# Kernel tuning notes

Hardware: AMD Instinct MI355X
Metric: run time of the kernel (lower is better)

The kernel has to match this reference:

```python
import jax, jax.numpy as jnp
import numpy as np

# Action space: 3 discrete action types, 8 options each (MultiDiscrete nvec)
ACTION_NUMS = np.array([8, 8, 8])
A_TOTAL = int(ACTION_NUMS.sum())          # 24
START_IDX = np.cumsum([0, *ACTION_NUMS[:-1]])  # [0, 8, 16]
F, N, D = 4096, 64, 256                   # frames, agents(actions per frame), feat_size
HID = 140                                 # fixed in ForwardNet


def setup_inputs() -> dict:
    key = jax.random.key(0)
    ks = jax.random.split(key, 8)
    s = lambda fan_in: 1.0 / np.sqrt(fan_in)
    return {
        "current_feature": jax.random.normal(ks[0], (F, N, D), jnp.float32),
        "next_feature": jax.random.normal(ks[1], (F, N, D), jnp.float32),
        "actions": jax.random.randint(ks[2], (F, 3, N), 0, 8, dtype=jnp.int32),
        "W1": jax.random.normal(ks[3], (D + A_TOTAL, HID), jnp.float32) * s(D + A_TOTAL),
        "b1": jnp.zeros((HID,), jnp.float32),
        "W2": jax.random.normal(ks[4], (HID, D), jnp.float32) * s(HID),
        "b2": jnp.zeros((D,), jnp.float32),
        "Wi": jax.random.normal(ks[5], (2 * D, A_TOTAL), jnp.float32) * s(2 * D),
        "bi": jnp.zeros((A_TOTAL,), jnp.float32),
    }


def actions2onehot(actions):
    # actions: [F, T, N] int. Vectorized replacement for the triple Python loop:
    # each (frame, agent) row gets a 1 at START_IDX[type] + action, per type.
    start = jnp.asarray(START_IDX, actions.dtype)          # [T]
    idx = actions + start[None, :, None]                    # [F, T, N]
    oh = jax.nn.one_hot(idx, A_TOTAL, dtype=jnp.float32)    # [F, T, N, A]
    return oh.sum(axis=1)                                   # [F, N, A] (column ranges disjoint)


def reference(current_feature, next_feature, actions, W1, b1, W2, b2, Wi, bi):
    action_one_hot = actions2onehot(actions)                       # [F, N, 24]
    # Forward dynamics (attn_target != ICM branch)
    fwd_in = jnp.concatenate([current_feature, action_one_hot], axis=2)  # [F, N, 280]
    h = jax.nn.leaky_relu(fwd_in @ W1 + b1, negative_slope=0.1)
    next_feature_pred = h @ W2 + b2                                # [F, N, 256]
    # Inverse dynamics
    inv_in = jnp.concatenate([current_feature, next_feature], axis=2)   # [F, N, 512]
    action_pred = inv_in @ Wi + bi                                 # [F, N, 24] per-type logits concatenated
    return next_feature_pred, action_pred
```

## Files before the change

kernel.cpp:

```cpp
#include <hip/hip_runtime.h>
#include <hip/hip_bf16.h>
#include <stdint.h>


typedef __attribute__((ext_vector_type(8))) short short8;
typedef __attribute__((ext_vector_type(4))) float float4v;

#define MFMA16 __builtin_amdgcn_mfma_f32_16x16x32_bf16

__device__ __align__(16) uint16_t g_wpack[98816];

__device__ __forceinline__ void gl_lds16(const void* g, void* l) {
    __builtin_amdgcn_global_load_lds(
        (const __attribute__((address_space(1))) unsigned int*)g,
        (__attribute__((address_space(3))) unsigned int*)l, 16, 0, 0);
}

__device__ __forceinline__ uint16_t f2bf(float f) {
    __hip_bfloat16 h = __float2bfloat16(f);
    return *reinterpret_cast<uint16_t*>(&h);
}

__device__ __forceinline__ short8 cvt8(float4v x0, float4v x1) {
    union { __hip_bfloat162 b2[4]; short8 s; } u;
    u.b2[0] = __float22bfloat162_rn(make_float2(x0[0], x0[1]));
    u.b2[1] = __float22bfloat162_rn(make_float2(x0[2], x0[3]));
    u.b2[2] = __float22bfloat162_rn(make_float2(x1[0], x1[1]));
    u.b2[3] = __float22bfloat162_rn(make_float2(x1[2], x1[3]));
    return u.s;
}

__global__ __launch_bounds__(256) void pack_weights(
    const float* __restrict__ W1, const float* __restrict__ W2,
    const float* __restrict__ Wi)
{
    int e = blockIdx.x * 256 + threadIdx.x;
    const float* W; int NT, Kr, Nr, ld, le, base;
    if (e < 41472)      { W = W1; NT = 9;  Kr = 280; Nr = 140; ld = 140; le = e;         base = 0; }
    else if (e < 82432) { W = W2; NT = 16; Kr = 140; Nr = 256; ld = 256; le = e - 41472; base = 41472; }
    else if (e < 98816) { W = Wi; NT = 2;  Kr = 512; Nr = 24;  ld = 24;  le = e - 82432; base = 82432; }
    else return;
    int i = le & 7, lane = (le >> 3) & 63, frag = le >> 9;
    int kt = frag / NT, nt = frag - kt * NT;
    int k = kt * 32 + ((lane >> 4) << 3) + i;
    int n = nt * 16 + (lane & 15);
    float v = (k < Kr && n < Nr) ? W[k * ld + n] : 0.0f;
    g_wpack[base + le] = f2bf(v);
}

__global__ __launch_bounds__(256, 2) void icm_main(
    const float* __restrict__ cf, const float* __restrict__ nf,
    const int* __restrict__ act,
    const float* __restrict__ b1, const float* __restrict__ b2,
    const float* __restrict__ bi,
    float* __restrict__ out)
{
    __shared__ char smem[73728];

    const int tid  = threadIdx.x;
    const int wave = tid >> 6;
    const int lane = tid & 63;
    const int lhi  = lane >> 4;
    const int llo  = lane & 15;
    char* hA   = smem + wave * 8192;
    char* hB   = smem + 32768 + wave * 2048;
    char* wstA = smem + 40960;
    char* wstB = smem + 57344;

    const long rowbase = (long)blockIdx.x * 128 + wave * 32;
    const char* gw = (const char*)g_wpack;

    auto stage1 = [&](char* dst, int kt) {
        const char* w1b = gw + kt * 9216;
        const char* wib = gw + 164864 + kt * 2048;
        const int nb = (kt == 8) ? 9216 : 11264;
        #pragma unroll
        for (int k = 0; k < 3; ++k) {
            int b = k * 4096 + wave * 1024;
            if (b < nb) {
                const char* src = (b < 9216) ? (w1b + b) : (wib + (b - 9216));
                gl_lds16(src + lane * 16, dst + b);
            }
        }
    };
    auto stage16 = [&](char* dst, const char* src) {
        #pragma unroll
        for (int k = 0; k < 4; ++k) {
            int b = k * 4096 + wave * 1024;
            gl_lds16(src + b + lane * 16, dst + b);
        }
    };

    int i0[2], i1[2], i2[2];
    #pragma unroll
    for (int m = 0; m < 2; ++m) {
        long r = rowbase + m * 16 + llo;
        long f = r >> 6; int n = (int)(r & 63);
        i0[m] = act[(f * 3 + 0) * 64 + n];
        i1[m] = act[(f * 3 + 1) * 64 + n] + 8;
        i2[m] = act[(f * 3 + 2) * 64 + n] + 16;
    }
    float bb1[9];
    #pragma unroll
    for (int nt = 0; nt < 9; ++nt) {
        int col = nt * 16 + llo;
        bb1[nt] = b1[col < 140 ? col : 139];
    }
    float bi0 = bi[llo];
    float bi1 = (llo < 8) ? bi[16 + llo] : 0.f;

    const float4v fz = {0.f, 0.f, 0.f, 0.f};
    float4v acc1[2][9];
    float4v acc3[2][2];
    #pragma unroll
    for (int m = 0; m < 2; ++m) {
        #pragma unroll
        for (int n = 0; n < 9; ++n) acc1[m][n] = fz;
        acc3[m][0] = fz; acc3[m][1] = fz;
    }

    const float* cfb[2];
    #pragma unroll
    for (int m = 0; m < 2; ++m)
        cfb[m] = cf + (rowbase + m * 16 + llo) * 256 + lhi * 8;

    float4v pa0[2], pa1[2], pb0[2], pb1[2];
    stage1(wstA, 0);
    #pragma unroll
    for (int m = 0; m < 2; ++m) {
        pa0[m] = *(const float4v*)(cfb[m]);
        pa1[m] = *(const float4v*)(cfb[m] + 4);
        pb0[m] = *(const float4v*)(cfb[m] + 32);
        pb1[m] = *(const float4v*)(cfb[m] + 36);
    }
    __syncthreads();

    #pragma unroll 1
    for (int kt = 0; kt < 8; ++kt) {
        stage1((kt & 1) ? wstA : wstB, kt + 1);
        const char* wb = (kt & 1) ? wstB : wstA;
        short8 a[2];
        if (kt & 1) { a[0] = cvt8(pb0[0], pb1[0]); a[1] = cvt8(pb0[1], pb1[1]); }
        else        { a[0] = cvt8(pa0[0], pa1[0]); a[1] = cvt8(pa0[1], pa1[1]); }
        if (kt <= 5) {
            int o = (kt + 2) * 32;
            if (kt & 1) {
                #pragma unroll
                for (int m = 0; m < 2; ++m) {
                    pb0[m] = *(const float4v*)(cfb[m] + o);
                    pb1[m] = *(const float4v*)(cfb[m] + o + 4);
                }
            } else {
                #pragma unroll
                for (int m = 0; m < 2; ++m) {
                    pa0[m] = *(const float4v*)(cfb[m] + o);
                    pa1[m] = *(const float4v*)(cfb[m] + o + 4);
                }
            }
        }
        #pragma unroll
        for (int nt = 0; nt < 9; ++nt) {
            short8 bf = *(const short8*)(wb + (nt << 10) + (lane << 4));
            acc1[0][nt] = MFMA16(a[0], bf, acc1[0][nt], 0, 0, 0);
            acc1[1][nt] = MFMA16(a[1], bf, acc1[1][nt], 0, 0, 0);
        }
        #pragma unroll
        for (int nt = 0; nt < 2; ++nt) {
            short8 bf = *(const short8*)(wb + ((9 + nt) << 10) + (lane << 4));
            acc3[0][nt] = MFMA16(a[0], bf, acc3[0][nt], 0, 0, 0);
            acc3[1][nt] = MFMA16(a[1], bf, acc3[1][nt], 0, 0, 0);
        }
        __syncthreads();
    }
    {
        short8 a[2];
        #pragma unroll
        for (int m = 0; m < 2; ++m) {
            #pragma unroll
            for (int i = 0; i < 8; ++i) {
                int kk = lhi * 8 + i;
                a[m][i] = (kk == i0[m] || kk == i1[m] || kk == i2[m])
                              ? (short)0x3F80 : (short)0;
            }
        }
        #pragma unroll
        for (int nt = 0; nt < 9; ++nt) {
            short8 bf = *(const short8*)(wstA + (nt << 10) + (lane << 4));
            acc1[0][nt] = MFMA16(a[0], bf, acc1[0][nt], 0, 0, 0);
            acc1[1][nt] = MFMA16(a[1], bf, acc1[1][nt], 0, 0, 0);
        }
    }
    __syncthreads();

    stage16(wstB, gw + 164864 + 16384);
    stage16(wstA, gw + 82944);

    #pragma unroll
    for (int m = 0; m < 2; ++m) {
        #pragma unroll
        for (int nt = 0; nt < 9; ++nt) {
            int col = nt * 16 + llo;
            #pragma unroll
            for (int r = 0; r < 4; ++r) {
                float v = acc1[m][nt][r] + bb1[nt];
                v = v > 0.f ? v : 0.1f * v;
                int row = m * 16 + lhi * 4 + r;
                if (nt < 8) {
                    int off = row * 256 + ((col * 2) ^ ((row & 7) << 4));
                    *(uint16_t*)(hA + off) = f2bf(v);
                } else {
                    int off = row * 64 + (((col - 128) * 2) ^ ((row & 3) << 4));
                    *(uint16_t*)(hB + off) = f2bf(v);
                }
            }
        }
    }
    #pragma unroll
    for (int z = 0; z < 4; ++z) {
        int zz  = lane * 4 + z;
        int row = zz >> 3, d = zz & 7;
        int off = row * 64 + ((32 + d * 4) ^ ((row & 3) << 4));
        *(int*)(hB + off) = 0;
    }

    const float* nfb[2];
    #pragma unroll
    for (int m = 0; m < 2; ++m)
        nfb[m] = nf + (rowbase + m * 16 + llo) * 256 + lhi * 8;
    #pragma unroll
    for (int m = 0; m < 2; ++m) {
        pa0[m] = *(const float4v*)(nfb[m]);
        pa1[m] = *(const float4v*)(nfb[m] + 4);
        pb0[m] = *(const float4v*)(nfb[m] + 32);
        pb1[m] = *(const float4v*)(nfb[m] + 36);
    }
    __syncthreads();

    #pragma unroll 1
    for (int kt = 0; kt < 8; ++kt) {
        short8 a[2];
        if (kt & 1) { a[0] = cvt8(pb0[0], pb1[0]); a[1] = cvt8(pb0[1], pb1[1]); }
        else        { a[0] = cvt8(pa0[0], pa1[0]); a[1] = cvt8(pa0[1], pa1[1]); }
        if (kt <= 5) {
            int o = (kt + 2) * 32;
            if (kt & 1) {
                #pragma unroll
                for (int m = 0; m < 2; ++m) {
                    pb0[m] = *(const float4v*)(nfb[m] + o);
                    pb1[m] = *(const float4v*)(nfb[m] + o + 4);
                }
            } else {
                #pragma unroll
                for (int m = 0; m < 2; ++m) {
                    pa0[m] = *(const float4v*)(nfb[m] + o);
                    pa1[m] = *(const float4v*)(nfb[m] + o + 4);
                }
            }
        }
        #pragma unroll
        for (int nt = 0; nt < 2; ++nt) {
            short8 bf = *(const short8*)(wstB + (((kt << 1) + nt) << 10) + (lane << 4));
            acc3[0][nt] = MFMA16(a[0], bf, acc3[0][nt], 0, 0, 0);
            acc3[1][nt] = MFMA16(a[1], bf, acc3[1][nt], 0, 0, 0);
        }
    }
    float* out2 = out + 67108864L;
    #pragma unroll
    for (int m = 0; m < 2; ++m) {
        #pragma unroll
        for (int nt = 0; nt < 2; ++nt) {
            int col = nt * 16 + llo;
            if (col < 24) {
                float bb = (nt == 0) ? bi0 : bi1;
                #pragma unroll
                for (int r = 0; r < 4; ++r) {
                    long row = rowbase + m * 16 + lhi * 4 + r;
                    out2[row * 24 + col] = acc3[m][nt][r] + bb;
                }
            }
        }
    }
    __syncthreads();

    float4v acc2[2][16];
    #pragma unroll
    for (int m = 0; m < 2; ++m)
        #pragma unroll
        for (int n = 0; n < 16; ++n) acc2[m][n] = fz;

    #pragma unroll 1
    for (int kt = 0; kt < 5; ++kt) {
        if (kt < 4) stage16((kt & 1) ? wstA : wstB, gw + 82944 + (kt + 1) * 16384);
        const char* wb = (kt & 1) ? wstB : wstA;
        short8 a[2];
        #pragma unroll
        for (int m = 0; m < 2; ++m) {
            int row = m * 16 + llo;
            if (kt < 4) {
                int off = row * 256 + ((kt * 64 + lhi * 16) ^ ((row & 7) << 4));
                a[m] = *(const short8*)(hA + off);
            } else {
                int off = row * 64 + ((lhi * 16) ^ ((row & 3) << 4));
                a[m] = *(const short8*)(hB + off);
            }
        }
        #pragma unroll
        for (int nt = 0; nt < 16; ++nt) {
            short8 bf = *(const short8*)(wb + (nt << 10) + (lane << 4));
            acc2[0][nt] = MFMA16(a[0], bf, acc2[0][nt], 0, 0, 0);
            acc2[1][nt] = MFMA16(a[1], bf, acc2[1][nt], 0, 0, 0);
        }
        if (kt < 4) __syncthreads();
    }

    #pragma unroll
    for (int m = 0; m < 2; ++m) {
        #pragma unroll
        for (int n = 0; n < 16; ++n) {
            int col = n * 16 + llo;
            float bb = b2[col];
            #pragma unroll
            for (int r = 0; r < 4; ++r) {
                long row = rowbase + m * 16 + lhi * 4 + r;
                out[row * 256 + col] = acc2[m][n][r] + bb;
            }
        }
    }
}

extern "C" void kernel_launch(void* const* d_in, const int* in_sizes, int n_in,
                              void* d_out, int out_size, void* d_ws, size_t ws_size,
                              hipStream_t stream) {
    const float *cf = nullptr, *nf = nullptr, *W1 = nullptr, *b1 = nullptr;
    const float *W2 = nullptr, *b2 = nullptr, *Wi = nullptr, *bi = nullptr;
    const int *ac = nullptr;
    for (int i = 0; i < n_in; ++i) {
        int s = in_sizes[i];
        const void* p = d_in[i];
        switch (s) {
            case 67108864: if (!cf) cf = (const float*)p; else nf = (const float*)p; break;
            case 786432:   ac = (const int*)p;   break;
            case 39200:    W1 = (const float*)p; break;
            case 140:      b1 = (const float*)p; break;
            case 35840:    W2 = (const float*)p; break;
            case 256:      b2 = (const float*)p; break;
            case 12288:    Wi = (const float*)p; break;
            case 24:       bi = (const float*)p; break;
            default: break;
        }
    }
    float* ob = (float*)d_out;

    pack_weights<<<386, 256, 0, stream>>>(W1, W2, Wi);
    icm_main<<<2048, 256, 0, stream>>>(cf, nf, ac, b1, b2, bi, ob);
}
```

Before: 201.0 us.

## Keep hidden activations in registers via operand swap and bpermute, shrink LDS

The first GEMM now computes the transposed product by swapping MFMA operands, so each lane holds hidden activations along K. After bias and leaky-relu, results are packed to bf16 in registers and moved with ds_bpermute into the A-fragment layout for the second GEMM. This removes the per-wave LDS staging of the hidden layer. The second GEMM is split into two 128-column halves with 8KB weight stages, cutting LDS to 22KB and raising the occupancy target to 3 blocks. The cost is more register pressure, extra bpermute traffic, and twice as many weight-stage barriers.

```diff
diff --git a/kernel.cpp b/kernel.cpp
--- a/kernel.cpp
+++ b/kernel.cpp
@@ -10,18 +10,23 @@
 
 __device__ __align__(16) uint16_t g_wpack[98816];
 
-__device__ __forceinline__ void gl_lds16(const void* g, void* l) {
+static __device__ __forceinline__ void gl_lds16(const void* g, void* l) {
     __builtin_amdgcn_global_load_lds(
         (const __attribute__((address_space(1))) unsigned int*)g,
         (__attribute__((address_space(3))) unsigned int*)l, 16, 0, 0);
 }
 
-__device__ __forceinline__ uint16_t f2bf(float f) {
+static __device__ __forceinline__ uint16_t f2bf(float f) {
     __hip_bfloat16 h = __float2bfloat16(f);
     return *reinterpret_cast<uint16_t*>(&h);
 }
 
-__device__ __forceinline__ short8 cvt8(float4v x0, float4v x1) {
+static __device__ __forceinline__ int pk2(float lo, float hi) {
+    __hip_bfloat162 b = __float22bfloat162_rn(make_float2(lo, hi));
+    int u; __builtin_memcpy(&u, &b, 4); return u;
+}
+
+static __device__ __forceinline__ short8 cvt8(float4v x0, float4v x1) {
     union { __hip_bfloat162 b2[4]; short8 s; } u;
     u.b2[0] = __float22bfloat162_rn(make_float2(x0[0], x0[1]));
     u.b2[1] = __float22bfloat162_rn(make_float2(x0[2], x0[3]));
@@ -48,24 +53,22 @@
     g_wpack[base + le] = f2bf(v);
 }
 
-__global__ __launch_bounds__(256, 2) void icm_main(
+__global__ __launch_bounds__(256, 3) void icm_main(
     const float* __restrict__ cf, const float* __restrict__ nf,
     const int* __restrict__ act,
     const float* __restrict__ b1, const float* __restrict__ b2,
     const float* __restrict__ bi,
     float* __restrict__ out)
 {
-    __shared__ char smem[73728];
+    __shared__ char smem[22528];
+    char* wstA = smem;
+    char* wstB = smem + 11264;
 
     const int tid  = threadIdx.x;
+    const int lane = tid & 63;
     const int wave = tid >> 6;
-    const int lane = tid & 63;
     const int lhi  = lane >> 4;
     const int llo  = lane & 15;
-    char* hA   = smem + wave * 8192;
-    char* hB   = smem + 32768 + wave * 2048;
-    char* wstA = smem + 40960;
-    char* wstB = smem + 57344;
 
     const long rowbase = (long)blockIdx.x * 128 + wave * 32;
     const char* gw = (const char*)g_wpack;
@@ -83,9 +86,9 @@
             }
         }
     };
-    auto stage16 = [&](char* dst, const char* src) {
-        #pragma unroll
-        for (int k = 0; k < 4; ++k) {
+    auto stage8 = [&](char* dst, const char* src) {
+        #pragma unroll
+        for (int k = 0; k < 2; ++k) {
             int b = k * 4096 + wave * 1024;
             gl_lds16(src + b + lane * 16, dst + b);
         }
@@ -99,12 +102,6 @@
         i0[m] = act[(f * 3 + 0) * 64 + n];
         i1[m] = act[(f * 3 + 1) * 64 + n] + 8;
         i2[m] = act[(f * 3 + 2) * 64 + n] + 16;
-    }
-    float bb1[9];
-    #pragma unroll
-    for (int nt = 0; nt < 9; ++nt) {
-        int col = nt * 16 + llo;
-        bb1[nt] = b1[col < 140 ? col : 139];
     }
     float bi0 = bi[llo];
     float bi1 = (llo < 8) ? bi[16 + llo] : 0.f;
@@ -161,8 +158,8 @@
         #pragma unroll
         for (int nt = 0; nt < 9; ++nt) {
             short8 bf = *(const short8*)(wb + (nt << 10) + (lane << 4));
-            acc1[0][nt] = MFMA16(a[0], bf, acc1[0][nt], 0, 0, 0);
-            acc1[1][nt] = MFMA16(a[1], bf, acc1[1][nt], 0, 0, 0);
+            acc1[0][nt] = MFMA16(bf, a[0], acc1[0][nt], 0, 0, 0);
+            acc1[1][nt] = MFMA16(bf, a[1], acc1[1][nt], 0, 0, 0);
         }
         #pragma unroll
         for (int nt = 0; nt < 2; ++nt) {
@@ -186,41 +183,29 @@
         #pragma unroll
         for (int nt = 0; nt < 9; ++nt) {
             short8 bf = *(const short8*)(wstA + (nt << 10) + (lane << 4));
-            acc1[0][nt] = MFMA16(a[0], bf, acc1[0][nt], 0, 0, 0);
-            acc1[1][nt] = MFMA16(a[1], bf, acc1[1][nt], 0, 0, 0);
-        }
-    }
-    __syncthreads();
-
-    stage16(wstB, gw + 164864 + 16384);
-    stage16(wstA, gw + 82944);
-
-    #pragma unroll
-    for (int m = 0; m < 2; ++m) {
-        #pragma unroll
-        for (int nt = 0; nt < 9; ++nt) {
-            int col = nt * 16 + llo;
-            #pragma unroll
-            for (int r = 0; r < 4; ++r) {
-                float v = acc1[m][nt][r] + bb1[nt];
-                v = v > 0.f ? v : 0.1f * v;
-                int row = m * 16 + lhi * 4 + r;
-                if (nt < 8) {
-                    int off = row * 256 + ((col * 2) ^ ((row & 7) << 4));
-                    *(uint16_t*)(hA + off) = f2bf(v);
-                } else {
-                    int off = row * 64 + (((col - 128) * 2) ^ ((row & 3) << 4));
-                    *(uint16_t*)(hB + off) = f2bf(v);
-                }
-            }
-        }
-    }
-    #pragma unroll
-    for (int z = 0; z < 4; ++z) {
-        int zz  = lane * 4 + z;
-        int row = zz >> 3, d = zz & 7;
-        int off = row * 64 + ((32 + d * 4) ^ ((row & 3) << 4));
-        *(int*)(hB + off) = 0;
+            acc1[0][nt] = MFMA16(bf, a[0], acc1[0][nt], 0, 0, 0);
+            acc1[1][nt] = MFMA16(bf, a[1], acc1[1][nt], 0, 0, 0);
+        }
+    }
+    __syncthreads();
+
+    stage8(wstA, gw + 164864 + 16384);
+    stage8(wstB, gw + 164864 + 24576);
+
+    int w01[2][9], w23[2][9];
+    #pragma unroll
+    for (int nt = 0; nt < 9; ++nt) {
+        int bb = nt * 16 + lhi * 4; bb = bb > 136 ? 136 : bb;
+        float4v b1v = *(const float4v*)(b1 + bb);
+        #pragma unroll
+        for (int m = 0; m < 2; ++m) {
+            float v0 = acc1[m][nt][0] + b1v[0]; v0 = v0 > 0.f ? v0 : 0.1f * v0;
+            float v1 = acc1[m][nt][1] + b1v[1]; v1 = v1 > 0.f ? v1 : 0.1f * v1;
+            float v2 = acc1[m][nt][2] + b1v[2]; v2 = v2 > 0.f ? v2 : 0.1f * v2;
+            float v3 = acc1[m][nt][3] + b1v[3]; v3 = v3 > 0.f ? v3 : 0.1f * v3;
+            w01[m][nt] = pk2(v0, v1);
+            w23[m][nt] = pk2(v2, v3);
+        }
     }
 
     const float* nfb[2];
@@ -259,7 +244,9 @@
         }
         #pragma unroll
         for (int nt = 0; nt < 2; ++nt) {
-            short8 bf = *(const short8*)(wstB + (((kt << 1) + nt) << 10) + (lane << 4));
+            int f = 2 * kt + nt;
+            const char* bse = smem + ((f & 8) ? 11264 : 0) + ((f & 7) << 10);
+            short8 bf = *(const short8*)(bse + (lane << 4));
             acc3[0][nt] = MFMA16(a[0], bf, acc3[0][nt], 0, 0, 0);
             acc3[1][nt] = MFMA16(a[1], bf, acc3[1][nt], 0, 0, 0);
         }
@@ -282,47 +269,76 @@
     }
     __syncthreads();
 
-    float4v acc2[2][16];
-    #pragma unroll
-    for (int m = 0; m < 2; ++m)
-        #pragma unroll
-        for (int n = 0; n < 16; ++n) acc2[m][n] = fz;
+    stage8(wstA, gw + 82944);
+
+    short8 hfrag[2][5];
+    {
+        int addrA = ((lane & 15) + ((lane & 16) ? 32 : 0)) * 4;
+        int addrB = addrA + 64;
+        bool hisel = (lane & 32) != 0;
+        #pragma unroll
+        for (int m = 0; m < 2; ++m) {
+            #pragma unroll
+            for (int kt = 0; kt < 5; ++kt) {
+                const int j0 = 2 * kt;
+                const int j1 = (2 * kt + 1 > 8) ? 8 : (2 * kt + 1);
+                int u0 = w01[m][j0], u1 = w23[m][j0];
+                int u2 = w01[m][j1], u3 = w23[m][j1];
+                int a0 = __builtin_amdgcn_ds_bpermute(addrA, u0);
+                int a2 = __builtin_amdgcn_ds_bpermute(addrA, u2);
+                int b0 = __builtin_amdgcn_ds_bpermute(addrA, u1);
+                int b2 = __builtin_amdgcn_ds_bpermute(addrA, u3);
+                int c0 = __builtin_amdgcn_ds_bpermute(addrB, u0);
+                int c2 = __builtin_amdgcn_ds_bpermute(addrB, u2);
+                int e0 = __builtin_amdgcn_ds_bpermute(addrB, u1);
+                int e2 = __builtin_amdgcn_ds_bpermute(addrB, u3);
+                union { int d[4]; short8 s; } t;
+                t.d[0] = hisel ? a2 : a0;
+                t.d[1] = hisel ? b2 : b0;
+                t.d[2] = hisel ? c2 : c0;
+                t.d[3] = hisel ? e2 : e0;
+                hfrag[m][kt] = t.s;
+            }
+        }
+    }
+    __syncthreads();
 
     #pragma unroll 1
-    for (int kt = 0; kt < 5; ++kt) {
-        if (kt < 4) stage16((kt & 1) ? wstA : wstB, gw + 82944 + (kt + 1) * 16384);
-        const char* wb = (kt & 1) ? wstB : wstA;
-        short8 a[2];
+    for (int p = 0; p < 2; ++p) {
+        float4v acc2[2][8];
+        #pragma unroll
+        for (int m = 0; m < 2; ++m)
+            #pragma unroll
+            for (int n = 0; n < 8; ++n) acc2[m][n] = fz;
+
+        #pragma unroll
+        for (int kt = 0; kt < 5; ++kt) {
+            int q = p * 5 + kt;
+            if (q < 9) {
+                int qn = q + 1;
+                int off = ((qn >= 5 ? qn - 5 : qn) * 16 + (qn >= 5 ? 8 : 0)) << 10;
+                stage8((q & 1) ? wstA : wstB, gw + 82944 + off);
+            }
+            const char* wb = (q & 1) ? wstB : wstA;
+            #pragma unroll
+            for (int n = 0; n < 8; ++n) {
+                short8 bf = *(const short8*)(wb + (n << 10) + (lane << 4));
+                acc2[0][n] = MFMA16(hfrag[0][kt], bf, acc2[0][n], 0, 0, 0);
+                acc2[1][n] = MFMA16(hfrag[1][kt], bf, acc2[1][n], 0, 0, 0);
+            }
+            if (q < 9) __syncthreads();
+        }
         #pragma unroll
         for (int m = 0; m < 2; ++m) {
-            int row = m * 16 + llo;
-            if (kt < 4) {
-                int off = row * 256 + ((kt * 64 + lhi * 16) ^ ((row & 7) << 4));
-                a[m] = *(const short8*)(hA + off);
-            } else {
-                int off = row * 64 + ((lhi * 16) ^ ((row & 3) << 4));
-                a[m] = *(const short8*)(hB + off);
-            }
-        }
-        #pragma unroll
-        for (int nt = 0; nt < 16; ++nt) {
-            short8 bf = *(const short8*)(wb + (nt << 10) + (lane << 4));
-            acc2[0][nt] = MFMA16(a[0], bf, acc2[0][nt], 0, 0, 0);
-            acc2[1][nt] = MFMA16(a[1], bf, acc2[1][nt], 0, 0, 0);
-        }
-        if (kt < 4) __syncthreads();
-    }
-
-    #pragma unroll
-    for (int m = 0; m < 2; ++m) {
-        #pragma unroll
-        for (int n = 0; n < 16; ++n) {
-            int col = n * 16 + llo;
-            float bb = b2[col];
-            #pragma unroll
-            for (int r = 0; r < 4; ++r) {
-                long row = rowbase + m * 16 + lhi * 4 + r;
-                out[row * 256 + col] = acc2[m][n][r] + bb;
+            #pragma unroll
+            for (int n = 0; n < 8; ++n) {
+                int col = (p * 8 + n) * 16 + llo;
+                float bb = b2[col];
+                #pragma unroll
+                for (int r = 0; r < 4; ++r) {
+                    long row = rowbase + m * 16 + lhi * 4 + r;
+                    out[row * 256 + col] = acc2[m][n][r] + bb;
+                }
             }
         }
     }
```

Result: slower. 266.3 us (+32.5%).
